# Optimization experiments

Measured on AMD Instinct MI355X. Metric: run time of the kernel, lower is better.

Reference implementation:

```python
import jax, jax.numpy as jnp
import numpy as np

WS = 8          # window size
DIM = 192
NH = 6          # num heads
HD = DIM // NH  # head dim = 32
HIDDEN = 768    # mlp_ratio 4
EPS = 1e-5


def _rel_tables(ws):
    # continuous relative-coords table, shape (1, 2w-1, 2w-1, 2)
    r = np.arange(-(ws - 1), ws, dtype=np.float32)
    table = np.stack(np.meshgrid(r, r, indexing='ij'), axis=-1)[None]
    table = table / (ws - 1) * 8.0
    # relative position index, shape (N, N)
    coords = np.stack(np.meshgrid(np.arange(ws), np.arange(ws), indexing='ij'))
    cf = coords.reshape(2, -1)
    rel = (cf[:, :, None] - cf[:, None, :]).transpose(1, 2, 0).astype(np.int64)
    rel[:, :, 0] += ws - 1
    rel[:, :, 1] += ws - 1
    rel[:, :, 0] *= 2 * ws - 1
    idx = rel.sum(-1)
    return jnp.asarray(table), jnp.asarray(idx)

_TABLE, _RPI = _rel_tables(WS)


def _layernorm(x, g, b):
    m = jnp.mean(x, -1, keepdims=True)
    v = jnp.var(x, -1, keepdims=True)
    return (x - m) * jax.lax.rsqrt(v + EPS) * g + b


def setup_inputs() -> dict:
    key = jax.random.key(0)
    ks = jax.random.split(key, 12)
    B, H, W = 2, 256, 256
    s = 0.02
    return {
        'x': jax.random.normal(ks[0], (B, H * W, DIM), jnp.float32),
        'scale': jax.random.uniform(ks[1], (1, 2), jnp.float32, 0.5, 2.0),
        'norm1_g': jnp.ones((DIM,), jnp.float32),
        'norm1_b': jnp.zeros((DIM,), jnp.float32),
        'qkv_w': jax.random.normal(ks[2], (DIM, 3 * DIM), jnp.float32) * s,
        'qkv_b': jnp.zeros((3 * DIM,), jnp.float32),
        'proj_w': jax.random.normal(ks[3], (DIM, DIM), jnp.float32) * s,
        'proj_b': jnp.zeros((DIM,), jnp.float32),
        'cpb_w1': jax.random.normal(ks[4], (4, 512), jnp.float32) * s,
        'cpb_b1': jnp.zeros((512,), jnp.float32),
        'cpb_w2': jax.random.normal(ks[5], (512, NH), jnp.float32) * s,
        'cpb_b2': jnp.zeros((NH,), jnp.float32),
        'norm2_g': jnp.ones((DIM,), jnp.float32),
        'norm2_b': jnp.zeros((DIM,), jnp.float32),
        'fc1_w': jax.random.normal(ks[6], (DIM, HIDDEN), jnp.float32) * s,
        'fc1_b': jnp.zeros((HIDDEN,), jnp.float32),
        'fc2_w': jax.random.normal(ks[7], (HIDDEN, DIM), jnp.float32) * s,
        'fc2_b': jnp.zeros((DIM,), jnp.float32),
        'dw_w': jax.random.normal(ks[8], (HIDDEN, 1, 3, 3), jnp.float32) * s,
        'dw_b': jnp.zeros((HIDDEN,), jnp.float32),
        'H': 256,
        'W': 256,
    }


def reference(x, scale, norm1_g, norm1_b, qkv_w, qkv_b, proj_w, proj_b,
              cpb_w1, cpb_b1, cpb_w2, cpb_b2, norm2_g, norm2_b,
              fc1_w, fc1_b, fc2_w, fc2_b, dw_w, dw_b, H, W):
    B, L, C = x.shape
    N = WS * WS
    shortcut = x

    # ---- W-MSA branch ----
    h = _layernorm(x, norm1_g, norm1_b).reshape(B, H, W, C)
    # window partition -> (B*nW, N, C)
    h = h.reshape(B, H // WS, WS, W // WS, WS, C).transpose(0, 1, 3, 2, 4, 5)
    xw = h.reshape(-1, N, C)
    B_ = xw.shape[0]

    qkv = (xw @ qkv_w + qkv_b).reshape(B_, N, 3, NH, HD).transpose(2, 0, 3, 1, 4)
    q, k, v = qkv[0], qkv[1], qkv[2]          # (B_, NH, N, HD)
    q = q * (HD ** -0.5)
    attn = jnp.einsum('bhnd,bhmd->bhnm', q, k)  # (B_, NH, N, N)

    # continuous relative position bias from cpb MLP conditioned on `scale`
    rel_cell = jnp.broadcast_to(scale[:, None, None, :], _TABLE.shape)  # (1,2w-1,2w-1,2)
    coords4 = jnp.concatenate([_TABLE, rel_cell], axis=-1)              # (1,2w-1,2w-1,4)
    bias_tab = (jax.nn.relu(coords4 @ cpb_w1 + cpb_b1) @ cpb_w2 + cpb_b2).reshape(-1, NH)
    rpb = bias_tab[_RPI.reshape(-1)].reshape(N, N, NH).transpose(2, 0, 1)  # (NH,N,N)
    attn = jax.nn.softmax(attn + rpb[None], axis=-1)

    out = jnp.einsum('bhnm,bhmd->bhnd', attn, v).transpose(0, 2, 1, 3).reshape(B_, N, C)
    out = out @ proj_w + proj_b

    # window reverse
    out = out.reshape(B, H // WS, W // WS, WS, WS, C).transpose(0, 1, 3, 2, 4, 5)
    out = out.reshape(B, L, C)
    x = shortcut + out

    # ---- conv-augmented MLP branch ----
    h = _layernorm(x, norm2_g, norm2_b)
    h = jax.nn.gelu(h @ fc1_w + fc1_b, approximate=False)   # (B, L, HIDDEN)
    hc = h.transpose(0, 2, 1).reshape(B, HIDDEN, H, W)
    hc = jax.lax.conv_general_dilated(
        hc, dw_w, window_strides=(1, 1), padding=((1, 1), (1, 1)),
        dimension_numbers=('NCHW', 'OIHW', 'NCHW'), feature_group_count=HIDDEN)
    hc = hc + dw_b[None, :, None, None]
    h = hc.reshape(B, HIDDEN, L).transpose(0, 2, 1)
    h = jax.nn.gelu(h, approximate=False)
    h = h @ fc2_w + fc2_b
    return x + h
```

## Files before the change

### kernel.cpp

```cpp
#include <hip/hip_runtime.h>
#include <hip/hip_bf16.h>

typedef __attribute__((ext_vector_type(8))) short  bf16x8;
typedef __attribute__((ext_vector_type(4))) float  f32x4;
typedef __attribute__((ext_vector_type(8))) unsigned short u16x8;
typedef __attribute__((ext_vector_type(4))) unsigned short u16x4;

__device__ __forceinline__ unsigned short f2b(float f) {
    unsigned int u = __builtin_bit_cast(unsigned int, f);
    u += 0x7FFFu + ((u >> 16) & 1u);
    return (unsigned short)(u >> 16);
}
__device__ __forceinline__ float b2f(unsigned short u) {
    return __builtin_bit_cast(float, (unsigned int)u << 16);
}
__device__ __forceinline__ float gelu_fast(float x) {
    float d = 1.0f + __expf(-1.702f * x);
    return x * __builtin_amdgcn_rcpf(d);
}
__device__ __forceinline__ int wperm(int m) {
    int w = m >> 6, n = m & 63;
    int b = w >> 10, wy = (w >> 5) & 31, wx = w & 31;
    int y = wy * 8 + (n >> 3), xx = wx * 8 + (n & 7);
    return (b << 16) + (y << 8) + xx;
}

__device__ __forceinline__ void gload_lds16(const void* g, void* l) {
    __builtin_amdgcn_global_load_lds(
        (const __attribute__((address_space(1))) void*)g,
        (__attribute__((address_space(3))) void*)l, 16, 0, 0);
}

__global__ void transpose_w(const float* __restrict__ in, unsigned short* __restrict__ out,
                            int K, int N) {
    int i = blockIdx.x * 256 + threadIdx.x;
    if (i >= K * N) return;
    int n = i / K, k = i - n * K;
    out[i] = f2b(in[k * N + n]);
}

__global__ void transpose_wf(const float* __restrict__ in, float* __restrict__ out,
                             int K, int N) {
    int i = blockIdx.x * 256 + threadIdx.x;
    if (i >= K * N) return;
    int n = i / K, k = i - n * K;
    out[i] = in[k * N + n];
}

__global__ __launch_bounds__(256) void cpb_kernel(
    const float* __restrict__ scale, const float* __restrict__ w1, const float* __restrict__ b1,
    const float* __restrict__ w2, const float* __restrict__ b2, float* __restrict__ btab) {
    int t = threadIdx.x;
    if (t >= 225) return;
    int i = t / 15, j = t - (t / 15) * 15;
    float ti = (i - 7) * (8.0f / 7.0f);
    float tj = (j - 7) * (8.0f / 7.0f);
    float s0 = scale[0], s1 = scale[1];
    float acc[6];
    #pragma unroll
    for (int h = 0; h < 6; ++h) acc[h] = b2[h];
    for (int k = 0; k < 512; ++k) {
        float hv = ti * w1[k] + tj * w1[512 + k] + s0 * w1[1024 + k] + s1 * w1[1536 + k] + b1[k];
        hv = fmaxf(hv, 0.f);
        #pragma unroll
        for (int h = 0; h < 6; ++h) acc[h] += hv * w2[k * 6 + h];
    }
    #pragma unroll
    for (int h = 0; h < 6; ++h) btab[t * 6 + h] = acc[h];
}

template<int MODE>
__global__ __launch_bounds__(256) void gemm64(
    const float* __restrict__ Af, const unsigned short* __restrict__ Ab,
    const float* __restrict__ stats, const float* __restrict__ lng, const float* __restrict__ lnb,
    const unsigned short* __restrict__ Bt, const float* __restrict__ bias,
    unsigned short* __restrict__ oq, unsigned short* __restrict__ ok2, unsigned short* __restrict__ ov,
    const float* __restrict__ resid, float* __restrict__ ofp, unsigned short* __restrict__ obf,
    float* __restrict__ ostat) {
    constexpr int NCT = (MODE == 0) ? 3 : (MODE == 2) ? 4 : 1;
    __shared__ __align__(16) unsigned short Asw[3 * 64 * 64];
    __shared__ __align__(16) unsigned short Bsw[2 * 192 * 64];
    const int t = threadIdx.x, lane = t & 63, wv = t >> 6;
    const int wm = wv >> 1, wn = wv & 1;
    const int l15 = lane & 15, lq = lane >> 4;
    const int m0 = blockIdx.x * 64;

    int boffs[6];
    #pragma unroll
    for (int s = 0; s < 6; ++s) {
        int row = (wv + 4 * s) * 8 + (lane >> 3);
        boffs[s] = row * 192 + ((lane & 7) ^ (lane >> 3)) * 8;
    }
    if constexpr (MODE == 1) {
        #pragma unroll
        for (int s = 0; s < 6; ++s) {
            int si = wv + 4 * s;
            int row = (si & 7) * 8 + (lane >> 3);
            int src = (m0 + row) * 192 + (si >> 3) * 64 + ((lane & 7) ^ (lane >> 3)) * 8;
            gload_lds16(Ab + src, (char*)Asw + si * 1024);
        }
    }
    #pragma unroll
    for (int s = 0; s < 6; ++s)
        gload_lds16(Bt + boffs[s], (char*)Bsw + (wv + 4 * s) * 1024);

    if constexpr (MODE == 0) {
        int row = t >> 2, qtr = t & 3;
        const float* p = Af + (size_t)wperm(m0 + row) * 192 + qtr * 48;
        f32x4 v[12];
        float s = 0.f, q = 0.f;
        #pragma unroll
        for (int i = 0; i < 12; ++i) {
            v[i] = *(const f32x4*)(p + i * 4);
            #pragma unroll
            for (int j = 0; j < 4; ++j) { s += v[i][j]; q += v[i][j] * v[i][j]; }
        }
        s += __shfl_xor(s, 1); s += __shfl_xor(s, 2);
        q += __shfl_xor(q, 1); q += __shfl_xor(q, 2);
        float mean = s * (1.f / 192.f);
        float rstd = rsqrtf(q * (1.f / 192.f) - mean * mean + 1e-5f);
        #pragma unroll
        for (int i = 0; i < 12; ++i) {
            int k = qtr * 48 + i * 4;
            u16x4 pk;
            #pragma unroll
            for (int j = 0; j < 4; ++j)
                pk[j] = f2b((v[i][j] - mean) * rstd * lng[k + j] + lnb[k + j]);
            int cc = k >> 6, ch = (k >> 2) & 15;
            int byte = cc * 8192 + row * 128 +
                       ((((ch >> 1) ^ (row & 7)) << 4) + ((ch & 1) << 3));
            *(u16x4*)((char*)Asw + byte) = pk;
        }
        asm volatile("s_waitcnt lgkmcnt(0)" ::: "memory");
    }
    if constexpr (MODE == 2) {
        #pragma unroll
        for (int c = 0; c < 3; ++c) {
            #pragma unroll
            for (int i = 0; i < 4; ++i) {
                int c2 = t + i * 256;
                int row = c2 >> 4, ch = c2 & 15;
                int m = m0 + row;
                f32x4 v = *(const f32x4*)(Af + (size_t)m * 192 + c * 64 + ch * 4);
                float mean = stats[2 * m], rstd = stats[2 * m + 1];
                u16x4 pk;
                #pragma unroll
                for (int j = 0; j < 4; ++j) {
                    int kk = c * 64 + ch * 4 + j;
                    pk[j] = f2b((v[j] - mean) * rstd * lng[kk] + lnb[kk]);
                }
                int byte = c * 8192 + row * 128 +
                           ((((ch >> 1) ^ (row & 7)) << 4) + ((ch & 1) << 3));
                *(u16x4*)((char*)Asw + byte) = pk;
            }
        }
        asm volatile("s_waitcnt lgkmcnt(0)" ::: "memory");
    }

    const int axor = (l15 & 7) << 4;
    int cur = 0, it = 0;
    for (int ct = 0; ct < NCT; ++ct) {
        f32x4 acc[2][6];
        #pragma unroll
        for (int i = 0; i < 2; ++i)
            #pragma unroll
            for (int j = 0; j < 6; ++j) acc[i][j] = (f32x4){0.f, 0.f, 0.f, 0.f};
        for (int c = 0; c < 3; ++c, ++it) {
            if (it < NCT * 3 - 1) {
                int ctn = (c == 2) ? ct + 1 : ct;
                int cn  = (c == 2) ? 0 : c + 1;
                #pragma unroll
                for (int s = 0; s < 6; ++s)
                    gload_lds16(Bt + (size_t)ctn * 36864 + boffs[s] + cn * 64,
                                (char*)Bsw + (cur ^ 1) * 24576 + (wv + 4 * s) * 1024);
                asm volatile("s_waitcnt vmcnt(6)" ::: "memory");
            } else {
                asm volatile("s_waitcnt vmcnt(0)" ::: "memory");
            }
            __builtin_amdgcn_sched_barrier(0);
            __builtin_amdgcn_s_barrier();
            __builtin_amdgcn_sched_barrier(0);
            const char* Al = (const char*)Asw + c * 8192;
            const char* Bl = (const char*)Bsw + cur * 24576;
            #pragma unroll
            for (int kk = 0; kk < 2; ++kk) {
                bf16x8 a[2], bb[6];
                #pragma unroll
                for (int mt = 0; mt < 2; ++mt)
                    a[mt] = *(const bf16x8*)(Al + (wm * 32 + mt * 16 + l15) * 128 +
                                             ((kk << 6) ^ (lq << 4) ^ axor));
                #pragma unroll
                for (int nt = 0; nt < 6; ++nt)
                    bb[nt] = *(const bf16x8*)(Bl + (wn * 96 + nt * 16 + l15) * 128 +
                                              ((kk << 6) ^ (lq << 4) ^ axor));
                #pragma unroll
                for (int mt = 0; mt < 2; ++mt)
                    #pragma unroll
                    for (int nt = 0; nt < 6; ++nt)
                        acc[mt][nt] = __builtin_amdgcn_mfma_f32_16x16x32_bf16(a[mt], bb[nt], acc[mt][nt], 0, 0, 0);
            }
            __builtin_amdgcn_sched_barrier(0);
            __builtin_amdgcn_s_barrier();
            cur ^= 1;
        }
        if constexpr (MODE == 0) {
            unsigned short* dst = (ct == 0) ? oq : (ct == 1) ? ok2 : ov;
            float qs = (ct == 0) ? 0.17677669529663689f : 1.0f;
            #pragma unroll
            for (int mt = 0; mt < 2; ++mt)
                #pragma unroll
                for (int nt = 0; nt < 6; ++nt)
                    #pragma unroll
                    for (int r = 0; r < 4; ++r) {
                        int m = m0 + wm * 32 + mt * 16 + lq * 4 + r;
                        int col = wn * 96 + nt * 16 + l15;
                        float v = (acc[mt][nt][r] + bias[ct * 192 + col]) * qs;
                        int head = col >> 5, d = col & 31;
                        int w = m >> 6, n = m & 63;
                        dst[((size_t)(w * 6 + head) * 64 + n) * 32 + d] = f2b(v);
                    }
        } else if constexpr (MODE == 2) {
            #pragma unroll
            for (int mt = 0; mt < 2; ++mt)
                #pragma unroll
                for (int nt = 0; nt < 6; ++nt)
                    #pragma unroll
                    for (int r = 0; r < 4; ++r) {
                        int m = m0 + wm * 32 + mt * 16 + lq * 4 + r;
                        int col = wn * 96 + nt * 16 + l15;
                        obf[(size_t)m * 768 + ct * 192 + col] =
                            f2b(gelu_fast(acc[mt][nt][r] + bias[ct * 192 + col]));
                    }
        } else {
            float* ls  = (float*)Asw;
            float* lsq = ls + 128;
            #pragma unroll
            for (int mt = 0; mt < 2; ++mt) {
                #pragma unroll
                for (int r = 0; r < 4; ++r) {
                    int lrow = wm * 32 + mt * 16 + lq * 4 + r;
                    int m = m0 + lrow;
                    int r2 = wperm(m);
                    float s = 0.f, q = 0.f;
                    #pragma unroll
                    for (int nt = 0; nt < 6; ++nt) {
                        int col = wn * 96 + nt * 16 + l15;
                        size_t idx = (size_t)r2 * 192 + col;
                        float w = resid[idx] + acc[mt][nt][r] + bias[col];
                        ofp[idx] = w;
                        s += w;
                        q += w * w;
                    }
                    #pragma unroll
                    for (int off = 1; off < 16; off <<= 1) {
                        s += __shfl_xor(s, off);
                        q += __shfl_xor(q, off);
                    }
                    if (l15 == 0) {
                        ls[lrow * 2 + wn] = s;
                        lsq[lrow * 2 + wn] = q;
                    }
                }
            }
            __syncthreads();
            if (t < 64) {
                float s = ls[t * 2] + ls[t * 2 + 1];
                float q = lsq[t * 2] + lsq[t * 2 + 1];
                float mean = s * (1.f / 192.f);
                float var = q * (1.f / 192.f) - mean * mean;
                int r2 = wperm(m0 + t);
                ostat[2 * r2] = mean;
                ostat[2 * r2 + 1] = rsqrtf(var + 1e-5f);
            }
        }
    }
}

__global__ __launch_bounds__(64) void attn_win(
    const unsigned short* __restrict__ qb, const unsigned short* __restrict__ kb,
    const unsigned short* __restrict__ vb, const float* __restrict__ btab,
    unsigned short* __restrict__ ao) {
    __shared__ float sb[225];
    __shared__ __align__(16) unsigned short pl[64 * 72];
    __shared__ __align__(16) unsigned short vT[32 * 72];
    const int bid = blockIdx.x;
    const int w = bid / 6, h = bid - w * 6;
    const int lane = threadIdx.x;
    const int l15 = lane & 15, lq = lane >> 4;

    for (int i = lane; i < 225; i += 64) sb[i] = btab[i * 6 + h];

    const unsigned short* qp = qb + (size_t)bid * 2048;
    const unsigned short* kp = kb + (size_t)bid * 2048;
    const unsigned short* vp = vb + (size_t)bid * 2048;

    bf16x8 qf[4], kf[4];
    #pragma unroll
    for (int i = 0; i < 4; ++i) {
        qf[i] = *(const bf16x8*)(qp + (i * 16 + l15) * 32 + lq * 8);
        kf[i] = *(const bf16x8*)(kp + (i * 16 + l15) * 32 + lq * 8);
    }
    #pragma unroll
    for (int i = 0; i < 4; ++i) {
        int c = lane + i * 64;
        int mr = c >> 2, d0 = (c & 3) * 8;
        u16x8 v = *(const u16x8*)(vp + mr * 32 + d0);
        #pragma unroll
        for (int j = 0; j < 8; ++j) vT[(d0 + j) * 72 + mr] = v[j];
    }
    f32x4 s[4][4];
    #pragma unroll
    for (int mt = 0; mt < 4; ++mt)
        #pragma unroll
        for (int nt = 0; nt < 4; ++nt)
            s[mt][nt] = __builtin_amdgcn_mfma_f32_16x16x32_bf16(
                qf[mt], kf[nt], (f32x4){0.f, 0.f, 0.f, 0.f}, 0, 0, 0);
    __syncthreads();
    #pragma unroll
    for (int mt = 0; mt < 4; ++mt) {
        #pragma unroll
        for (int r = 0; r < 4; ++r) {
            int n = mt * 16 + lq * 4 + r;
            int ny = n >> 3, nx = n & 7;
            float sv[4];
            float mx = -1e30f;
            #pragma unroll
            for (int nt = 0; nt < 4; ++nt) {
                int m = nt * 16 + l15;
                int idx = (ny - (m >> 3) + 7) * 15 + (nx - (m & 7) + 7);
                float val = s[mt][nt][r] + sb[idx];
                sv[nt] = val;
                mx = fmaxf(mx, val);
            }
            #pragma unroll
            for (int off = 1; off < 16; off <<= 1) mx = fmaxf(mx, __shfl_xor(mx, off));
            float sum = 0.f;
            #pragma unroll
            for (int nt = 0; nt < 4; ++nt) { sv[nt] = __expf(sv[nt] - mx); sum += sv[nt]; }
            #pragma unroll
            for (int off = 1; off < 16; off <<= 1) sum += __shfl_xor(sum, off);
            float inv = 1.f / sum;
            #pragma unroll
            for (int nt = 0; nt < 4; ++nt)
                pl[n * 72 + nt * 16 + l15] = f2b(sv[nt] * inv);
        }
    }
    __syncthreads();
    f32x4 o[4][2];
    #pragma unroll
    for (int i = 0; i < 4; ++i)
        #pragma unroll
        for (int j = 0; j < 2; ++j) o[i][j] = (f32x4){0.f, 0.f, 0.f, 0.f};
    #pragma unroll
    for (int mt = 0; mt < 4; ++mt)
        #pragma unroll
        for (int kk = 0; kk < 2; ++kk) {
            bf16x8 a = *(bf16x8*)&pl[(mt * 16 + l15) * 72 + kk * 32 + lq * 8];
            #pragma unroll
            for (int dt = 0; dt < 2; ++dt) {
                bf16x8 b = *(bf16x8*)&vT[(dt * 16 + l15) * 72 + kk * 32 + lq * 8];
                o[mt][dt] = __builtin_amdgcn_mfma_f32_16x16x32_bf16(a, b, o[mt][dt], 0, 0, 0);
            }
        }
    #pragma unroll
    for (int mt = 0; mt < 4; ++mt)
        #pragma unroll
        for (int dt = 0; dt < 2; ++dt)
            #pragma unroll
            for (int r = 0; r < 4; ++r) {
                int n = mt * 16 + lq * 4 + r;
                int d = dt * 16 + l15;
                ao[((size_t)w * 64 + n) * 192 + h * 32 + d] = f2b(o[mt][dt][r]);
            }
}

__global__ __launch_bounds__(512) void conv_fc2_v12(
    const unsigned short* __restrict__ m1, const float* __restrict__ dwwTf,
    const float* __restrict__ dwb, const unsigned short* __restrict__ fc2T,
    const float* __restrict__ fc2b, float* __restrict__ out) {
    __shared__ __align__(16) unsigned short Xs[4 * 34 * 64];
    __shared__ __align__(16) unsigned short As[64 * 72];
    __shared__ __align__(16) unsigned short Bsw[192 * 64];
    const int t = threadIdx.x;
    const int g = ((blockIdx.x & 7) << 8) + (blockIdx.x >> 3);
    const int b = g >> 10, ypair = (g >> 3) & 127, xq = g & 7;
    const int y0 = ypair * 2, x0 = xq * 32;
    const int cg = t & 7, lx = t >> 3;
    const int ix = lx & 31, iy = lx >> 5;
    const size_t ibase = (size_t)b * 65536;

    const int lane = t & 63, wv8 = t >> 6;
    const int wm = wv8 >> 2, wn = wv8 & 3;
    const int l15 = lane & 15, lq = lane >> 4;

    int xoff[3];
    #pragma unroll
    for (int s = 0; s < 3; ++s) {
        int seg = (s < 2) ? (wv8 + 8 * s) : 16;
        int p = seg * 8 + (lane >> 3);
        int ry = p / 34, px = p - ry * 34;
        int gy = min(max(y0 - 1 + ry, 0), 255);
        int gx = min(max(x0 - 1 + px, 0), 255);
        xoff[s] = ((b << 16) + (gy << 8) + gx) * 768 + (lane & 7) * 8;
    }
    int boff[3];
    #pragma unroll
    for (int s = 0; s < 3; ++s) {
        int row = (wv8 + 8 * s) * 8 + (lane >> 3);
        boff[s] = row * 768 + ((lane & 7) ^ (lane >> 3)) * 8;
    }

    f32x4 acc[2][3];
    #pragma unroll
    for (int i = 0; i < 2; ++i)
        #pragma unroll
        for (int j = 0; j < 3; ++j) acc[i][j] = (f32x4){0.f, 0.f, 0.f, 0.f};

    #pragma unroll
    for (int s = 0; s < 3; ++s)
        if (s < 2 || wv8 == 0)
            gload_lds16(m1 + xoff[s], (char*)Xs + (((s < 2) ? (wv8 + 8 * s) : 16)) * 1024);
    #pragma unroll
    for (int s = 0; s < 3; ++s)
        gload_lds16(fc2T + boff[s], (char*)Bsw + (wv8 + 8 * s) * 1024);

    const int xb = ix * 128 + cg * 16;
    const int gxp = x0 + ix;
    const bool xok0 = gxp >= 1;
    const bool xok2 = gxp <= 254;
    const int oy = y0 + iy;
    const int o00 = (lq * 16) ^ ((l15 & 7) << 4);
    const int brow = (wn * 48 + l15) * 128;

    for (int k0 = 0; k0 < 768; k0 += 64) {
        const int c0 = k0 + cg * 8;
        asm volatile("s_waitcnt vmcnt(0)" ::: "memory");
        __syncthreads();
        float a[8];
        #pragma unroll
        for (int j = 0; j < 8; ++j) a[j] = 0.f;
        #pragma unroll
        for (int ky = 0; ky < 3; ++ky) {
            if ((unsigned)(oy + ky - 1) >= 256u) continue;
            #pragma unroll
            for (int kx = 0; kx < 3; ++kx) {
                if (kx == 0 && !xok0) continue;
                if (kx == 2 && !xok2) continue;
                const float* wp = dwwTf + (ky * 3 + kx) * 768 + c0;
                f32x4 w0 = *(const f32x4*)wp;
                f32x4 w1 = *(const f32x4*)(wp + 4);
                u16x8 in = *(const u16x8*)((const char*)Xs + (iy + ky) * 4352 + xb + kx * 128);
                #pragma unroll
                for (int j = 0; j < 4; ++j) {
                    a[j]     += b2f(in[j]) * w0[j];
                    a[4 + j] += b2f(in[4 + j]) * w1[j];
                }
            }
        }
        {
            f32x4 b0 = *(const f32x4*)(dwb + c0);
            f32x4 b1 = *(const f32x4*)(dwb + c0 + 4);
            u16x8 o;
            #pragma unroll
            for (int j = 0; j < 4; ++j) {
                o[j]     = f2b(gelu_fast(a[j] + b0[j]));
                o[4 + j] = f2b(gelu_fast(a[4 + j] + b1[j]));
            }
            *(u16x8*)&As[lx * 72 + cg * 8] = o;
        }
        __syncthreads();
        if (k0 < 704) {
            #pragma unroll
            for (int s = 0; s < 3; ++s)
                if (s < 2 || wv8 == 0)
                    gload_lds16(m1 + xoff[s] + k0 + 64,
                                (char*)Xs + (((s < 2) ? (wv8 + 8 * s) : 16)) * 1024);
        }
        #pragma unroll
        for (int kk = 0; kk < 2; ++kk) {
            bf16x8 af[2];
            #pragma unroll
            for (int mt = 0; mt < 2; ++mt)
                af[mt] = *(bf16x8*)&As[(wm * 32 + mt * 16 + l15) * 72 + kk * 32 + lq * 8];
            #pragma unroll
            for (int nt = 0; nt < 3; ++nt) {
                bf16x8 bb = *(const bf16x8*)((const char*)Bsw + brow + nt * 2048 + (o00 ^ (kk << 6)));
                #pragma unroll
                for (int mt = 0; mt < 2; ++mt)
                    acc[mt][nt] = __builtin_amdgcn_mfma_f32_16x16x32_bf16(af[mt], bb, acc[mt][nt], 0, 0, 0);
            }
        }
        __syncthreads();
        if (k0 < 704) {
            #pragma unroll
            for (int s = 0; s < 3; ++s)
                gload_lds16(fc2T + boff[s] + k0 + 64, (char*)Bsw + (wv8 + 8 * s) * 1024);
        }
    }
    #pragma unroll
    for (int mt = 0; mt < 2; ++mt)
        #pragma unroll
        for (int nt = 0; nt < 3; ++nt)
            #pragma unroll
            for (int r = 0; r < 4; ++r) {
                int ml = wm * 32 + mt * 16 + lq * 4 + r;
                int py = ml >> 5, lxx = ml & 31;
                int col = wn * 48 + nt * 16 + l15;
                size_t idx = (ibase + (size_t)(y0 + py) * 256 + x0 + lxx) * 192 + col;
                out[idx] = out[idx] + acc[mt][nt][r] + fc2b[col];
            }
}

extern "C" void kernel_launch(void* const* d_in, const int* in_sizes, int n_in,
                              void* d_out, int out_size, void* d_ws, size_t ws_size,
                              hipStream_t stream) {
    (void)in_sizes; (void)n_in; (void)out_size; (void)ws_size;
    const float* x     = (const float*)d_in[0];
    const float* scale = (const float*)d_in[1];
    const float* n1g   = (const float*)d_in[2];
    const float* n1b   = (const float*)d_in[3];
    const float* qkvw  = (const float*)d_in[4];
    const float* qkvb  = (const float*)d_in[5];
    const float* projw = (const float*)d_in[6];
    const float* projb = (const float*)d_in[7];
    const float* cw1   = (const float*)d_in[8];
    const float* cb1   = (const float*)d_in[9];
    const float* cw2   = (const float*)d_in[10];
    const float* cb2   = (const float*)d_in[11];
    const float* n2g   = (const float*)d_in[12];
    const float* n2b   = (const float*)d_in[13];
    const float* fc1w  = (const float*)d_in[14];
    const float* fc1b  = (const float*)d_in[15];
    const float* fc2w  = (const float*)d_in[16];
    const float* fc2b  = (const float*)d_in[17];
    const float* dww   = (const float*)d_in[18];
    const float* dwb   = (const float*)d_in[19];
    float* out = (float*)d_out;

    char* ws = (char*)d_ws;
    unsigned short* qkvT  = (unsigned short*)ws;
    unsigned short* projT = qkvT + 110592;
    unsigned short* fc1T  = projT + 36864;
    unsigned short* fc2T  = fc1T + 147456;
    float* btab   = (float*)(ws + 1048576);
    float* dwwTf  = (float*)(ws + 1310720);
    float* stats  = (float*)(ws + 2097152);
    unsigned short* pool = (unsigned short*)(ws + 4194304);
    const size_t S = 25165824;
    unsigned short* qb = pool;
    unsigned short* kb = pool + S;
    unsigned short* vb = pool + 2 * S;
    unsigned short* ab = pool + 3 * S;
    unsigned short* m1 = pool;

    transpose_w<<<432, 256, 0, stream>>>(qkvw, qkvT, 192, 576);
    transpose_w<<<144, 256, 0, stream>>>(projw, projT, 192, 192);
    transpose_w<<<576, 256, 0, stream>>>(fc1w, fc1T, 192, 768);
    transpose_w<<<576, 256, 0, stream>>>(fc2w, fc2T, 768, 192);
    transpose_wf<<<27, 256, 0, stream>>>(dww, dwwTf, 768, 9);
    cpb_kernel<<<1, 256, 0, stream>>>(scale, cw1, cb1, cw2, cb2, btab);

    gemm64<0><<<2048, 256, 0, stream>>>(
        x, (const unsigned short*)nullptr, (const float*)nullptr, n1g, n1b,
        qkvT, qkvb,
        qb, kb, vb, (const float*)nullptr, (float*)nullptr, (unsigned short*)nullptr,
        (float*)nullptr);
    attn_win<<<12288, 64, 0, stream>>>(qb, kb, vb, btab, ab);
    gemm64<1><<<2048, 256, 0, stream>>>(
        (const float*)nullptr, ab, (const float*)nullptr, (const float*)nullptr,
        (const float*)nullptr, projT, projb,
        (unsigned short*)nullptr, (unsigned short*)nullptr, (unsigned short*)nullptr,
        x, out, (unsigned short*)nullptr, stats);
    gemm64<2><<<2048, 256, 0, stream>>>(
        out, (const unsigned short*)nullptr, stats, n2g, n2b, fc1T, fc1b,
        (unsigned short*)nullptr, (unsigned short*)nullptr, (unsigned short*)nullptr,
        (const float*)nullptr, (float*)nullptr, m1, (float*)nullptr);
    conv_fc2_v12<<<2048, 512, 0, stream>>>(m1, dwwTf, dwb, fc2T, fc2b, out);
}
```

Baseline: 599.2 us.

## Enlarge conv+fc2 tile to four rows to reuse halo and weights

The fused depthwise-conv + fc2 kernel now handles a 4x32 pixel tile (128 rows) per block instead of 2x32, which halves the grid to 1024 blocks. Each thread computes two output rows, so the depthwise weight loads are shared across them. The 6-row input halo covers 4 output rows instead of 4 halo rows covering 2, which cuts redundant m1 reads. Each fc2 B-tile load now feeds twice as many MFMAs, at the cost of more accumulator registers (2x6 per wave) and a larger LDS footprint, which may lower occupancy.

New measurement: 578.5 us. -3.5%, faster.

```diff
diff --git a/kernel.cpp b/kernel.cpp
--- a/kernel.cpp
+++ b/kernel.cpp
@@ -374,34 +374,37 @@
             }
 }
 
-__global__ __launch_bounds__(512) void conv_fc2_v12(
+__global__ __launch_bounds__(512) void conv_fc2_v14(
     const unsigned short* __restrict__ m1, const float* __restrict__ dwwTf,
     const float* __restrict__ dwb, const unsigned short* __restrict__ fc2T,
     const float* __restrict__ fc2b, float* __restrict__ out) {
-    __shared__ __align__(16) unsigned short Xs[4 * 34 * 64];
-    __shared__ __align__(16) unsigned short As[64 * 72];
+    __shared__ __align__(16) unsigned short Xs[26 * 512];
+    __shared__ __align__(16) unsigned short As[128 * 72];
     __shared__ __align__(16) unsigned short Bsw[192 * 64];
     const int t = threadIdx.x;
-    const int g = ((blockIdx.x & 7) << 8) + (blockIdx.x >> 3);
-    const int b = g >> 10, ypair = (g >> 3) & 127, xq = g & 7;
-    const int y0 = ypair * 2, x0 = xq * 32;
+    const int g = ((blockIdx.x & 7) << 7) + (blockIdx.x >> 3);
+    const int b = g >> 9, yt = (g >> 3) & 63, xq = g & 7;
+    const int y0 = yt * 4, x0 = xq * 32;
     const int cg = t & 7, lx = t >> 3;
-    const int ix = lx & 31, iy = lx >> 5;
+    const int xx = lx & 31, yy0 = lx >> 5;
     const size_t ibase = (size_t)b * 65536;
 
     const int lane = t & 63, wv8 = t >> 6;
-    const int wm = wv8 >> 2, wn = wv8 & 3;
+    const int wm = wv8 >> 1, wn = wv8 & 1;
     const int l15 = lane & 15, lq = lane >> 4;
 
-    int xoff[3];
-    #pragma unroll
-    for (int s = 0; s < 3; ++s) {
-        int seg = (s < 2) ? (wv8 + 8 * s) : 16;
-        int p = seg * 8 + (lane >> 3);
-        int ry = p / 34, px = p - ry * 34;
-        int gy = min(max(y0 - 1 + ry, 0), 255);
+    int xoff[4];
+    #pragma unroll
+    for (int s = 0; s < 4; ++s) {
+        int seg = wv8 + 8 * s;
+        int e = seg * 512 + lane * 8;
+        e = min(e, 13048);
+        int row = e / 2176;
+        int rem = e - row * 2176;
+        int px = rem >> 6, ch = rem & 63;
+        int gy = min(max(y0 - 1 + row, 0), 255);
         int gx = min(max(x0 - 1 + px, 0), 255);
-        xoff[s] = ((b << 16) + (gy << 8) + gx) * 768 + (lane & 7) * 8;
+        xoff[s] = ((b << 16) + (gy << 8) + gx) * 768 + ch;
     }
     int boff[3];
     #pragma unroll
@@ -410,71 +413,85 @@
         boff[s] = row * 768 + ((lane & 7) ^ (lane >> 3)) * 8;
     }
 
-    f32x4 acc[2][3];
+    f32x4 acc[2][6];
     #pragma unroll
     for (int i = 0; i < 2; ++i)
         #pragma unroll
-        for (int j = 0; j < 3; ++j) acc[i][j] = (f32x4){0.f, 0.f, 0.f, 0.f};
-
-    #pragma unroll
-    for (int s = 0; s < 3; ++s)
-        if (s < 2 || wv8 == 0)
-            gload_lds16(m1 + xoff[s], (char*)Xs + (((s < 2) ? (wv8 + 8 * s) : 16)) * 1024);
+        for (int j = 0; j < 6; ++j) acc[i][j] = (f32x4){0.f, 0.f, 0.f, 0.f};
+
+    #pragma unroll
+    for (int s = 0; s < 4; ++s)
+        if (wv8 + 8 * s < 26)
+            gload_lds16(m1 + xoff[s], (char*)Xs + (wv8 + 8 * s) * 1024);
     #pragma unroll
     for (int s = 0; s < 3; ++s)
         gload_lds16(fc2T + boff[s], (char*)Bsw + (wv8 + 8 * s) * 1024);
 
-    const int xb = ix * 128 + cg * 16;
-    const int gxp = x0 + ix;
+    const int xb = xx * 128 + cg * 16;
+    const int gxp = x0 + xx;
     const bool xok0 = gxp >= 1;
     const bool xok2 = gxp <= 254;
-    const int oy = y0 + iy;
+    const int oy0 = y0 + yy0;
     const int o00 = (lq * 16) ^ ((l15 & 7) << 4);
-    const int brow = (wn * 48 + l15) * 128;
+    const int brow = (wn * 96 + l15) * 128;
 
     for (int k0 = 0; k0 < 768; k0 += 64) {
         const int c0 = k0 + cg * 8;
         asm volatile("s_waitcnt vmcnt(0)" ::: "memory");
         __syncthreads();
-        float a[8];
-        #pragma unroll
-        for (int j = 0; j < 8; ++j) a[j] = 0.f;
-        #pragma unroll
-        for (int ky = 0; ky < 3; ++ky) {
-            if ((unsigned)(oy + ky - 1) >= 256u) continue;
-            #pragma unroll
-            for (int kx = 0; kx < 3; ++kx) {
-                if (kx == 0 && !xok0) continue;
-                if (kx == 2 && !xok2) continue;
+        float a0[8], a1[8];
+        #pragma unroll
+        for (int j = 0; j < 8; ++j) { a0[j] = 0.f; a1[j] = 0.f; }
+        #pragma unroll
+        for (int kx = 0; kx < 3; ++kx) {
+            if (kx == 0 && !xok0) continue;
+            if (kx == 2 && !xok2) continue;
+            #pragma unroll
+            for (int ky = 0; ky < 3; ++ky) {
                 const float* wp = dwwTf + (ky * 3 + kx) * 768 + c0;
                 f32x4 w0 = *(const f32x4*)wp;
                 f32x4 w1 = *(const f32x4*)(wp + 4);
-                u16x8 in = *(const u16x8*)((const char*)Xs + (iy + ky) * 4352 + xb + kx * 128);
-                #pragma unroll
-                for (int j = 0; j < 4; ++j) {
-                    a[j]     += b2f(in[j]) * w0[j];
-                    a[4 + j] += b2f(in[4 + j]) * w1[j];
+                if ((unsigned)(oy0 + ky - 1) < 256u) {
+                    u16x8 in = *(const u16x8*)((const char*)Xs +
+                        (yy0 + ky) * 4352 + xb + kx * 128);
+                    #pragma unroll
+                    for (int j = 0; j < 4; ++j) {
+                        a0[j]     += b2f(in[j]) * w0[j];
+                        a0[4 + j] += b2f(in[4 + j]) * w1[j];
+                    }
+                }
+                if ((unsigned)(oy0 + ky + 1) < 256u) {
+                    u16x8 in = *(const u16x8*)((const char*)Xs +
+                        (yy0 + 2 + ky) * 4352 + xb + kx * 128);
+                    #pragma unroll
+                    for (int j = 0; j < 4; ++j) {
+                        a1[j]     += b2f(in[j]) * w0[j];
+                        a1[4 + j] += b2f(in[4 + j]) * w1[j];
+                    }
                 }
             }
         }
         {
             f32x4 b0 = *(const f32x4*)(dwb + c0);
             f32x4 b1 = *(const f32x4*)(dwb + c0 + 4);
-            u16x8 o;
+            u16x8 o0, o1;
             #pragma unroll
             for (int j = 0; j < 4; ++j) {
-                o[j]     = f2b(gelu_fast(a[j] + b0[j]));
-                o[4 + j] = f2b(gelu_fast(a[4 + j] + b1[j]));
-            }
-            *(u16x8*)&As[lx * 72 + cg * 8] = o;
+                o0[j]     = f2b(gelu_fast(a0[j] + b0[j]));
+                o0[4 + j] = f2b(gelu_fast(a0[4 + j] + b1[j]));
+                o1[j]     = f2b(gelu_fast(a1[j] + b0[j]));
+                o1[4 + j] = f2b(gelu_fast(a1[4 + j] + b1[j]));
+            }
+            *(u16x8*)&As[lx * 72 + cg * 8] = o0;
+            *(u16x8*)&As[(lx + 64) * 72 + cg * 8] = o1;
         }
         __syncthreads();
         if (k0 < 704) {
             #pragma unroll
-            for (int s = 0; s < 3; ++s)
-                if (s < 2 || wv8 == 0)
+            for (int s = 0; s < 4; ++s)
+                if (wv8 + 8 * s < 26)
                     gload_lds16(m1 + xoff[s] + k0 + 64,
-                                (char*)Xs + (((s < 2) ? (wv8 + 8 * s) : 16)) * 1024);
+                                (char*)Xs + (wv8 + 8 * s) * 1024);
         }
         #pragma unroll
         for (int kk = 0; kk < 2; ++kk) {
@@ -483,7 +500,7 @@
             for (int mt = 0; mt < 2; ++mt)
                 af[mt] = *(bf16x8*)&As[(wm * 32 + mt * 16 + l15) * 72 + kk * 32 + lq * 8];
             #pragma unroll
-            for (int nt = 0; nt < 3; ++nt) {
+            for (int nt = 0; nt < 6; ++nt) {
                 bf16x8 bb = *(const bf16x8*)((const char*)Bsw + brow + nt * 2048 + (o00 ^ (kk << 6)));
                 #pragma unroll
                 for (int mt = 0; mt < 2; ++mt)
@@ -500,12 +517,12 @@
     #pragma unroll
     for (int mt = 0; mt < 2; ++mt)
         #pragma unroll
-        for (int nt = 0; nt < 3; ++nt)
+        for (int nt = 0; nt < 6; ++nt)
             #pragma unroll
             for (int r = 0; r < 4; ++r) {
                 int ml = wm * 32 + mt * 16 + lq * 4 + r;
                 int py = ml >> 5, lxx = ml & 31;
-                int col = wn * 48 + nt * 16 + l15;
+                int col = wn * 96 + nt * 16 + l15;
                 size_t idx = (ibase + (size_t)(y0 + py) * 256 + x0 + lxx) * 192 + col;
                 out[idx] = out[idx] + acc[mt][nt][r] + fc2b[col];
             }
@@ -575,5 +592,5 @@
         out, (const unsigned short*)nullptr, stats, n2g, n2b, fc1T, fc1b,
         (unsigned short*)nullptr, (unsigned short*)nullptr, (unsigned short*)nullptr,
         (const float*)nullptr, (float*)nullptr, m1, (float*)nullptr);
-    conv_fc2_v12<<<2048, 512, 0, stream>>>(m1, dwwTf, dwb, fc2T, fc2b, out);
-}
+    conv_fc2_v14<<<1024, 512, 0, stream>>>(m1, dwwTf, dwb, fc2T, fc2b, out);
+}
```
